# Kernel optimization log

Hardware: AMD Instinct MI355X
Metric: run time of the kernel (lower is better)

The kernel has to match this reference:

```python
import jax, jax.numpy as jnp
import numpy as np

N = 50000
E = 1600000
IN = 128
HID = 128
OUT = 64
NEG_SLOPE = 0.2  # DGL GATConv default leaky_relu slope


def _gat_layer(h, src, dst, W, al, ar, b, res=None, act=True):
    """DGL GATConv layer on an edge-list graph.
    h: [N, F_in]; W: [F_in, H*D]; al, ar, b: [H, D]; res: None | [N,H,D].
    Returns [N, H, D].
    """
    H, D = al.shape
    f = (h @ W).reshape(N, H, D)                      # fc projection
    el = jnp.sum(f * al, axis=-1)                     # [N, H]
    er = jnp.sum(f * ar, axis=-1)                     # [N, H]
    e = jax.nn.leaky_relu(el[src] + er[dst], NEG_SLOPE)  # [E, H]
    # edge softmax over incoming edges of each dst node
    m = jax.ops.segment_max(e, dst, num_segments=N)   # [N, H]
    ex = jnp.exp(e - m[dst])                          # [E, H]
    s = jax.ops.segment_sum(ex, dst, num_segments=N)  # [N, H]
    alpha = ex / s[dst]                               # [E, H]
    msg = f[src] * alpha[..., None]                   # [E, H, D]
    rst = jax.ops.segment_sum(msg, dst, num_segments=N)  # [N, H, D]
    if res is not None:
        rst = rst + res
    rst = rst + b                                     # bias [H, D] broadcast
    if act:
        rst = jax.nn.elu(rst)
    return rst


def setup_inputs() -> dict:
    key = jax.random.key(0)
    ks = jax.random.split(key, 16)
    x = jax.random.normal(ks[0], (N, IN), dtype=jnp.float32)
    src = jax.random.randint(ks[1], (E,), 0, N)
    dst = jax.random.randint(ks[2], (E,), 0, N)
    sc = 0.05
    # layer 0: IN -> 8 heads x 16, no residual, elu
    W0 = jax.random.normal(ks[3], (IN, 8 * 16), dtype=jnp.float32) * sc
    al0 = jax.random.normal(ks[4], (8, 16), dtype=jnp.float32) * sc
    ar0 = jax.random.normal(ks[5], (8, 16), dtype=jnp.float32) * sc
    b0 = jnp.zeros((8, 16), dtype=jnp.float32)
    # layer 1: HID -> 8 heads x 16, identity residual (HID == 8*16), elu
    W1 = jax.random.normal(ks[6], (HID, 8 * 16), dtype=jnp.float32) * sc
    al1 = jax.random.normal(ks[7], (8, 16), dtype=jnp.float32) * sc
    ar1 = jax.random.normal(ks[8], (8, 16), dtype=jnp.float32) * sc
    b1 = jnp.zeros((8, 16), dtype=jnp.float32)
    # layer 2: HID -> 1 head x 64, linear residual (128 != 64), no act
    W2 = jax.random.normal(ks[9], (HID, 1 * OUT), dtype=jnp.float32) * sc
    al2 = jax.random.normal(ks[10], (1, OUT), dtype=jnp.float32) * sc
    ar2 = jax.random.normal(ks[11], (1, OUT), dtype=jnp.float32) * sc
    b2 = jnp.zeros((1, OUT), dtype=jnp.float32)
    resW2 = jax.random.normal(ks[12], (HID, 1 * OUT), dtype=jnp.float32) * sc
    return {"x": x, "src": src, "dst": dst,
            "W0": W0, "al0": al0, "ar0": ar0, "b0": b0,
            "W1": W1, "al1": al1, "ar1": ar1, "b1": b1,
            "W2": W2, "al2": al2, "ar2": ar2, "b2": b2,
            "resW2": resW2}


def reference(x, src, dst, W0, al0, ar0, b0, W1, al1, ar1, b1,
              W2, al2, ar2, b2, resW2):
    # layer 0: no residual, elu, flatten heads (dropout=0)
    h = _gat_layer(x, src, dst, W0, al0, ar0, b0, res=None, act=True)
    h = h.reshape(N, -1)  # [N, 128]
    # layer 1: identity residual, elu, flatten heads
    res1 = h.reshape(N, 8, 16)
    h = _gat_layer(h, src, dst, W1, al1, ar1, b1, res=res1, act=True)
    h = h.reshape(N, -1)  # [N, 128]
    # layer 2: linear residual, no activation, mean over heads
    res2 = (h @ resW2).reshape(N, 1, OUT)
    h = _gat_layer(h, src, dst, W2, al2, ar2, b2, res=res2, act=False)
    return h.mean(axis=1)  # [N, 64]
```

## Files before the change

kernel.cpp:

```cpp
#include <hip/hip_runtime.h>
#include <hip/hip_fp16.h>
#include <math.h>


#define GN 50000
#define GE 1600000
#define NB 391
#define NBLK_A 512
#define CHUNK 3125

typedef _Float16 half8 __attribute__((ext_vector_type(8)));
typedef _Float16 half4v __attribute__((ext_vector_type(4)));
typedef float f32x4 __attribute__((ext_vector_type(4)));


__global__ __launch_bounds__(256) void bucketA(const int* __restrict__ dst, int* __restrict__ cnt) {
    __shared__ int hist[NB];
    for (int i = threadIdx.x; i < NB; i += 256) hist[i] = 0;
    __syncthreads();
    int b = blockIdx.x;
    int beg = b * CHUNK, end = beg + CHUNK;
    for (int i = beg + threadIdx.x; i < end; i += 256)
        atomicAdd(&hist[dst[i] >> 7], 1);
    __syncthreads();
    for (int k = threadIdx.x; k < NB; k += 256)
        cnt[k * NBLK_A + b] = hist[k];
}

__global__ __launch_bounds__(512) void bucketB(int* __restrict__ cnt, int* __restrict__ tot) {
    __shared__ int s[512];
    int k = blockIdx.x, t = threadIdx.x;
    int* row = cnt + k * NBLK_A;
    s[t] = row[t];
    __syncthreads();
    for (int ofs = 1; ofs < 512; ofs <<= 1) {
        int v = (t >= ofs) ? s[t - ofs] : 0;
        __syncthreads();
        s[t] += v;
        __syncthreads();
    }
    row[t] = (t == 0) ? 0 : s[t - 1];
    if (t == 511) tot[k] = s[511];
}

__global__ __launch_bounds__(512) void bucketB2(const int* __restrict__ tot, int* __restrict__ base,
                                                int* __restrict__ offs) {
    __shared__ int s[512];
    int t = threadIdx.x;
    s[t] = (t < NB) ? tot[t] : 0;
    __syncthreads();
    for (int ofs = 1; ofs < 512; ofs <<= 1) {
        int v = (t >= ofs) ? s[t - ofs] : 0;
        __syncthreads();
        s[t] += v;
        __syncthreads();
    }
    if (t <= NB) base[t] = (t == 0) ? 0 : s[t - 1];
    if (t == 0) offs[GN] = GE;
}

__global__ __launch_bounds__(256) void bucketC(const int* __restrict__ src, const int* __restrict__ dst,
                                               const int* __restrict__ cnt, const int* __restrict__ base,
                                               unsigned* __restrict__ ebuf) {
    __shared__ int cur[NB];
    int b = blockIdx.x;
    for (int k = threadIdx.x; k < NB; k += 256)
        cur[k] = base[k] + cnt[k * NBLK_A + b];
    __syncthreads();
    int beg = b * CHUNK, end = beg + CHUNK;
    for (int i = beg + threadIdx.x; i < end; i += 256) {
        int d = dst[i];
        int pos = atomicAdd(&cur[d >> 7], 1);
        ebuf[pos] = (unsigned)src[i] | ((unsigned)(d & 127) << 16);
    }
}

__global__ __launch_bounds__(256) void bucketD(const unsigned* __restrict__ ebuf, const int* __restrict__ base,
                                               int* __restrict__ offs, int* __restrict__ csrc) {
    __shared__ int hist[128], pre[128], cur[128];
    int k = blockIdx.x, t = threadIdx.x;
    if (t < 128) hist[t] = 0;
    __syncthreads();
    int lo = base[k], hi = base[k + 1];
    for (int i = lo + t; i < hi; i += 256)
        atomicAdd(&hist[ebuf[i] >> 16], 1);
    __syncthreads();
    if (t < 128) pre[t] = hist[t];
    __syncthreads();
    for (int ofs = 1; ofs < 128; ofs <<= 1) {
        int v = 0;
        if (t < 128 && t >= ofs) v = pre[t - ofs];
        __syncthreads();
        if (t < 128) pre[t] += v;
        __syncthreads();
    }
    if (t < 128) {
        int excl = (t == 0) ? 0 : pre[t - 1];
        cur[t] = lo + excl;
        int node = (k << 7) + t;
        if (node < GN) offs[node] = lo + excl;
    }
    __syncthreads();
    for (int i = lo + t; i < hi; i += 256) {
        unsigned v = ebuf[i];
        int pos = atomicAdd(&cur[v >> 16], 1);
        csrc[pos] = (int)(v & 0xFFFFu);
    }
}


__global__ __launch_bounds__(256) void wt_ker(const float* __restrict__ W, _Float16* __restrict__ WT, int N) {
    int i = blockIdx.x * 256 + threadIdx.x;
    if (i >= N * 128) return;
    int n = i >> 7, k = i & 127;
    WT[i] = (_Float16)W[k * N + n];
}

__global__ __launch_bounds__(256) void cvt_ker(const float4* __restrict__ X, __half2* __restrict__ Y, int n4) {
    int i = blockIdx.x * 256 + threadIdx.x;
    if (i >= n4) return;
    float4 v = X[i];
    Y[i * 2]     = __floats2half2_rn(v.x, v.y);
    Y[i * 2 + 1] = __floats2half2_rn(v.z, v.w);
}


template <int NT>
__global__ __launch_bounds__(256) void gemm_mfma(const _Float16* __restrict__ A,
                                                 const _Float16* __restrict__ WT,
                                                 _Float16* __restrict__ C, int nrows) {
    const int N = NT * 16;
    int wave = threadIdx.x >> 6;
    int lane = threadIdx.x & 63;
    int quad = lane >> 4;
    int l16 = lane & 15;
    int m = blockIdx.x * 64 + wave * 16 + l16;
    int mc = (m < nrows) ? m : (nrows - 1);
    const _Float16* ap = A + (size_t)mc * 128 + quad * 8;
    half8 a[4];
    #pragma unroll
    for (int kk = 0; kk < 4; ++kk) a[kk] = *(const half8*)(ap + kk * 32);
    f32x4 acc[NT];
    #pragma unroll
    for (int nt = 0; nt < NT; ++nt) acc[nt] = (f32x4){0.f, 0.f, 0.f, 0.f};
    const _Float16* wp = WT + (size_t)l16 * 128 + quad * 8;
    #pragma unroll
    for (int nt = 0; nt < NT; ++nt) {
        #pragma unroll
        for (int kk = 0; kk < 4; ++kk) {
            half8 b = *(const half8*)(wp + nt * 16 * 128 + kk * 32);
            acc[nt] = __builtin_amdgcn_mfma_f32_16x16x32_f16(a[kk], b, acc[nt], 0, 0, 0);
        }
    }
    int row0 = blockIdx.x * 64 + wave * 16 + quad * 4;
    #pragma unroll
    for (int nt = 0; nt < NT; ++nt) {
        #pragma unroll
        for (int r = 0; r < 4; ++r) {
            int row = row0 + r;
            if (row < nrows) C[(size_t)row * N + nt * 16 + l16] = (_Float16)acc[nt][r];
        }
    }
}


template <int H, int D>
__global__ __launch_bounds__(256) void attn_ker(const __half* __restrict__ f, const float* __restrict__ al,
                                                const float* __restrict__ ar, float* __restrict__ el,
                                                float* __restrict__ er, int total) {
    int i = blockIdx.x * 256 + threadIdx.x;
    if (i >= total) return;
    int h = i % H;
    const __half2* fp = (const __half2*)(f + (size_t)i * D);
    const float2* alp = (const float2*)(al + h * D);
    const float2* arp = (const float2*)(ar + h * D);
    float sl = 0.f, sr = 0.f;
    #pragma unroll
    for (int d = 0; d < D / 2; ++d) {
        float2 fv = __half22float2(fp[d]);
        float2 av = alp[d];
        float2 rv = arp[d];
        sl += fv.x * av.x + fv.y * av.y;
        sr += fv.x * rv.x + fv.y * rv.y;
    }
    el[i] = sl;
    er[i] = sr;
}


__global__ __launch_bounds__(256) void agg_multi(const int* __restrict__ offs, const int* __restrict__ csrc,
                                                 const _Float16* __restrict__ fh, const float* __restrict__ el,
                                                 const float* __restrict__ er, const float* __restrict__ bias,
                                                 const _Float16* __restrict__ resid, _Float16* __restrict__ out,
                                                 int n) {
    int node = blockIdx.x * 16 + (threadIdx.x >> 4);
    int lg = threadIdx.x & 15;
    if (node >= n) return;
    int head = lg >> 1;
    float ern = er[node * 8 + head];
    int beg = offs[node], end = offs[node + 1];
    float acc[8] = {};
    float ssum = 0.f;
    int e = beg;
    for (; e + 4 <= end; e += 4) {
        int s0 = csrc[e], s1 = csrc[e + 1], s2 = csrc[e + 2], s3 = csrc[e + 3];
        float e0 = el[s0 * 8 + head] + ern;
        float e1 = el[s1 * 8 + head] + ern;
        float e2 = el[s2 * 8 + head] + ern;
        float e3 = el[s3 * 8 + head] + ern;
        half8 q0 = *(const half8*)(fh + (size_t)s0 * 128 + lg * 8);
        half8 q1 = *(const half8*)(fh + (size_t)s1 * 128 + lg * 8);
        half8 q2 = *(const half8*)(fh + (size_t)s2 * 128 + lg * 8);
        half8 q3 = *(const half8*)(fh + (size_t)s3 * 128 + lg * 8);
        e0 = fmaxf(e0, 0.2f * e0);
        e1 = fmaxf(e1, 0.2f * e1);
        e2 = fmaxf(e2, 0.2f * e2);
        e3 = fmaxf(e3, 0.2f * e3);
        float w0 = __expf(e0), w1 = __expf(e1), w2 = __expf(e2), w3 = __expf(e3);
        ssum += (w0 + w1) + (w2 + w3);
        #pragma unroll
        for (int j = 0; j < 8; ++j)
            acc[j] += w0 * (float)q0[j] + w1 * (float)q1[j]
                    + w2 * (float)q2[j] + w3 * (float)q3[j];
    }
    for (; e < end; ++e) {
        int s = csrc[e];
        float ev = el[s * 8 + head] + ern;
        ev = fmaxf(ev, 0.2f * ev);
        float w = __expf(ev);
        half8 q = *(const half8*)(fh + (size_t)s * 128 + lg * 8);
        ssum += w;
        #pragma unroll
        for (int j = 0; j < 8; ++j) acc[j] += w * (float)q[j];
    }
    float inv = (ssum > 0.f) ? 1.0f / ssum : 0.f;
    float o[8];
    #pragma unroll
    for (int j = 0; j < 8; ++j) o[j] = acc[j] * inv + bias[lg * 8 + j];
    if (resid) {
        half8 r = *(const half8*)(resid + (size_t)node * 128 + lg * 8);
        #pragma unroll
        for (int j = 0; j < 8; ++j) o[j] += (float)r[j];
    }
    half8 ov;
    #pragma unroll
    for (int j = 0; j < 8; ++j) {
        float v = o[j];
        v = (v > 0.f) ? v : expm1f(v);
        ov[j] = (_Float16)v;
    }
    *(half8*)(out + (size_t)node * 128 + lg * 8) = ov;
}

__global__ __launch_bounds__(256) void agg_single(const int* __restrict__ offs, const int* __restrict__ csrc,
                                                  const _Float16* __restrict__ fh, const float* __restrict__ el,
                                                  const float* __restrict__ er, const float* __restrict__ bias,
                                                  const _Float16* __restrict__ resid, float* __restrict__ out,
                                                  int n) {
    int node = blockIdx.x * 16 + (threadIdx.x >> 4);
    int lg = threadIdx.x & 15;
    if (node >= n) return;
    float ern = er[node];
    int beg = offs[node], end = offs[node + 1];
    float acc[4] = {};
    float ssum = 0.f;
    int e = beg;
    for (; e + 4 <= end; e += 4) {
        int s0 = csrc[e], s1 = csrc[e + 1], s2 = csrc[e + 2], s3 = csrc[e + 3];
        float e0 = el[s0] + ern;
        float e1 = el[s1] + ern;
        float e2 = el[s2] + ern;
        float e3 = el[s3] + ern;
        half4v q0 = *(const half4v*)(fh + (size_t)s0 * 64 + lg * 4);
        half4v q1 = *(const half4v*)(fh + (size_t)s1 * 64 + lg * 4);
        half4v q2 = *(const half4v*)(fh + (size_t)s2 * 64 + lg * 4);
        half4v q3 = *(const half4v*)(fh + (size_t)s3 * 64 + lg * 4);
        e0 = fmaxf(e0, 0.2f * e0);
        e1 = fmaxf(e1, 0.2f * e1);
        e2 = fmaxf(e2, 0.2f * e2);
        e3 = fmaxf(e3, 0.2f * e3);
        float w0 = __expf(e0), w1 = __expf(e1), w2 = __expf(e2), w3 = __expf(e3);
        ssum += (w0 + w1) + (w2 + w3);
        #pragma unroll
        for (int j = 0; j < 4; ++j)
            acc[j] += w0 * (float)q0[j] + w1 * (float)q1[j]
                    + w2 * (float)q2[j] + w3 * (float)q3[j];
    }
    for (; e < end; ++e) {
        int s = csrc[e];
        float ev = el[s] + ern;
        ev = fmaxf(ev, 0.2f * ev);
        float w = __expf(ev);
        half4v q = *(const half4v*)(fh + (size_t)s * 64 + lg * 4);
        ssum += w;
        #pragma unroll
        for (int j = 0; j < 4; ++j) acc[j] += w * (float)q[j];
    }
    float inv = (ssum > 0.f) ? 1.0f / ssum : 0.f;
    half4v r = *(const half4v*)(resid + (size_t)node * 64 + lg * 4);
    float4 o;
    o.x = acc[0] * inv + bias[lg * 4 + 0] + (float)r[0];
    o.y = acc[1] * inv + bias[lg * 4 + 1] + (float)r[1];
    o.z = acc[2] * inv + bias[lg * 4 + 2] + (float)r[2];
    o.w = acc[3] * inv + bias[lg * 4 + 3] + (float)r[3];
    *(float4*)(out + (size_t)node * 64 + lg * 4) = o;
}


extern "C" void kernel_launch(void* const* d_in, const int* in_sizes, int n_in,
                              void* d_out, int out_size, void* d_ws, size_t ws_size,
                              hipStream_t stream) {
    const float* x     = (const float*)d_in[0];
    const int*   src   = (const int*)d_in[1];
    const int*   dst   = (const int*)d_in[2];
    const float* W0    = (const float*)d_in[3];
    const float* al0   = (const float*)d_in[4];
    const float* ar0   = (const float*)d_in[5];
    const float* b0    = (const float*)d_in[6];
    const float* W1    = (const float*)d_in[7];
    const float* al1   = (const float*)d_in[8];
    const float* ar1   = (const float*)d_in[9];
    const float* b1    = (const float*)d_in[10];
    const float* W2    = (const float*)d_in[11];
    const float* al2   = (const float*)d_in[12];
    const float* ar2   = (const float*)d_in[13];
    const float* b2    = (const float*)d_in[14];
    const float* resW2 = (const float*)d_in[15];
    float* out = (float*)d_out;

    char* w = (char*)d_ws;
    auto alloc = [&](size_t bytes) {
        char* p = w;
        w += (bytes + 255) & ~(size_t)255;
        return p;
    };
    int*      base  = (int*)alloc((size_t)(NB + 1) * 4);
    int*      offs  = (int*)alloc((size_t)(GN + 1) * 4);
    int*      csrc  = (int*)alloc((size_t)GE * 4);
    _Float16* fbuf  = (_Float16*)alloc((size_t)GN * 128 * 2);
    float*    elb   = (float*)alloc((size_t)GN * 8 * 4);
    float*    erb   = (float*)alloc((size_t)GN * 8 * 4);
    _Float16* x16   = (_Float16*)alloc((size_t)GN * 128 * 2);
    _Float16* hA    = (_Float16*)alloc((size_t)GN * 128 * 2);
    _Float16* hB    = (_Float16*)alloc((size_t)GN * 128 * 2);
    _Float16* res2  = (_Float16*)alloc((size_t)GN * 64 * 2);
    _Float16* w0t   = (_Float16*)alloc(128 * 128 * 2);
    _Float16* w1t   = (_Float16*)alloc(128 * 128 * 2);
    _Float16* w2t   = (_Float16*)alloc(64 * 128 * 2);
    _Float16* rw2t  = (_Float16*)alloc(64 * 128 * 2);

    int*      cnt  = (int*)hA;
    int*      tot  = (int*)hA + NB * NBLK_A;
    unsigned* ebuf = (unsigned*)hB;

    bucketA<<<NBLK_A, 256, 0, stream>>>(dst, cnt);
    bucketB<<<NB, 512, 0, stream>>>(cnt, tot);
    bucketB2<<<1, 512, 0, stream>>>(tot, base, offs);
    bucketC<<<NBLK_A, 256, 0, stream>>>(src, dst, cnt, base, ebuf);
    bucketD<<<NB, 256, 0, stream>>>(ebuf, base, offs, csrc);

    wt_ker<<<(128 * 128 + 255) / 256, 256, 0, stream>>>(W0, w0t, 128);
    wt_ker<<<(128 * 128 + 255) / 256, 256, 0, stream>>>(W1, w1t, 128);
    wt_ker<<<(64 * 128 + 255) / 256, 256, 0, stream>>>(W2, w2t, 64);
    wt_ker<<<(64 * 128 + 255) / 256, 256, 0, stream>>>(resW2, rw2t, 64);
    cvt_ker<<<(GN * 32 + 255) / 256, 256, 0, stream>>>((const float4*)x, (__half2*)x16, GN * 32);

    dim3 gblk(256);
    int gemmGrid = (GN + 63) / 64;
    int aggGrid = (GN + 15) / 16;

    gemm_mfma<8><<<gemmGrid, gblk, 0, stream>>>(x16, w0t, fbuf, GN);
    attn_ker<8, 16><<<(GN * 8 + 255) / 256, gblk, 0, stream>>>((const __half*)fbuf, al0, ar0, elb, erb, GN * 8);
    agg_multi<<<aggGrid, gblk, 0, stream>>>(offs, csrc, fbuf, elb, erb, b0, nullptr, hA, GN);

    gemm_mfma<8><<<gemmGrid, gblk, 0, stream>>>(hA, w1t, fbuf, GN);
    attn_ker<8, 16><<<(GN * 8 + 255) / 256, gblk, 0, stream>>>((const __half*)fbuf, al1, ar1, elb, erb, GN * 8);
    agg_multi<<<aggGrid, gblk, 0, stream>>>(offs, csrc, fbuf, elb, erb, b1, hA, hB, GN);

    gemm_mfma<4><<<gemmGrid, gblk, 0, stream>>>(hB, w2t, fbuf, GN);
    gemm_mfma<4><<<gemmGrid, gblk, 0, stream>>>(hB, rw2t, res2, GN);
    attn_ker<1, 64><<<(GN + 255) / 256, gblk, 0, stream>>>((const __half*)fbuf, al2, ar2, elb, erb, GN);
    agg_single<<<aggGrid, gblk, 0, stream>>>(offs, csrc, fbuf, elb, erb, b2, res2, out, GN);
}
```

Before: 402.9 us.

## Fuse attention-score computation and fp32 input conversion into MFMA projection GEMMs

Each layer's projection GEMM now also computes el/er with an extra MFMA. It stages the fp16 output tile in shared memory and multiplies it by a block-diagonal attention matrix built once in a combined prep kernel. Layer 0 reads fp32 x directly and converts it in registers, which drops the separate conversion pass and the x16 buffer. Layer 2's two GEMMs (projection and residual) share one A load in a dual variant. Together this removes several kernel launches and full re-reads of the feature buffers, at the cost of more LDS and registers per GEMM block and attention logits computed from fp16-rounded features and weights.

```diff
diff --git a/kernel.cpp b/kernel.cpp
--- a/kernel.cpp
+++ b/kernel.cpp
@@ -109,82 +109,145 @@
 }
 
 
-__global__ __launch_bounds__(256) void wt_ker(const float* __restrict__ W, _Float16* __restrict__ WT, int N) {
+__global__ __launch_bounds__(256) void prep(const float* __restrict__ W0, const float* __restrict__ W1,
+                                            const float* __restrict__ W2, const float* __restrict__ rW2,
+                                            const float* __restrict__ al0, const float* __restrict__ ar0,
+                                            const float* __restrict__ al1, const float* __restrict__ ar1,
+                                            const float* __restrict__ al2, const float* __restrict__ ar2,
+                                            _Float16* __restrict__ w0t, _Float16* __restrict__ w1t,
+                                            _Float16* __restrict__ w2t, _Float16* __restrict__ rw2t,
+                                            _Float16* __restrict__ aB0, _Float16* __restrict__ aB1,
+                                            _Float16* __restrict__ aB2) {
     int i = blockIdx.x * 256 + threadIdx.x;
-    if (i >= N * 128) return;
-    int n = i >> 7, k = i & 127;
-    WT[i] = (_Float16)W[k * N + n];
-}
-
-__global__ __launch_bounds__(256) void cvt_ker(const float4* __restrict__ X, __half2* __restrict__ Y, int n4) {
-    int i = blockIdx.x * 256 + threadIdx.x;
-    if (i >= n4) return;
-    float4 v = X[i];
-    Y[i * 2]     = __floats2half2_rn(v.x, v.y);
-    Y[i * 2 + 1] = __floats2half2_rn(v.z, v.w);
-}
-
-
-template <int NT>
-__global__ __launch_bounds__(256) void gemm_mfma(const _Float16* __restrict__ A,
-                                                 const _Float16* __restrict__ WT,
-                                                 _Float16* __restrict__ C, int nrows) {
+    if (i < 16384) {
+        int n = i >> 7, k = i & 127;
+        w0t[i] = (_Float16)W0[k * 128 + n];
+        w1t[i] = (_Float16)W1[k * 128 + n];
+    }
+    if (i < 8192) {
+        int n = i >> 7, k = i & 127;
+        w2t[i] = (_Float16)W2[k * 64 + n];
+        rw2t[i] = (_Float16)rW2[k * 64 + n];
+    }
+    if (i < 2048) {
+        int n = i >> 7, k = i & 127;
+        _Float16 v0 = (_Float16)0.f, v1 = (_Float16)0.f, v2 = (_Float16)0.f;
+        if (n < 8) {
+            if ((k >> 4) == n) {
+                v0 = (_Float16)al0[n * 16 + (k & 15)];
+                v1 = (_Float16)al1[n * 16 + (k & 15)];
+            }
+        } else {
+            int h = n - 8;
+            if ((k >> 4) == h) {
+                v0 = (_Float16)ar0[h * 16 + (k & 15)];
+                v1 = (_Float16)ar1[h * 16 + (k & 15)];
+            }
+        }
+        if (n == 0 && k < 64) v2 = (_Float16)al2[k];
+        if (n == 1 && k < 64) v2 = (_Float16)ar2[k];
+        aB0[i] = v0; aB1[i] = v1; aB2[i] = v2;
+    }
+}
+
+
+template <int NT, bool AF32, bool DUAL, bool MULTI>
+__global__ __launch_bounds__(256) void gemm_att(const void* __restrict__ Av,
+                                                const _Float16* __restrict__ WT,
+                                                const _Float16* __restrict__ WT2,
+                                                const _Float16* __restrict__ attB,
+                                                _Float16* __restrict__ C, _Float16* __restrict__ C2,
+                                                float* __restrict__ elb, float* __restrict__ erb,
+                                                int nrows) {
     const int N = NT * 16;
-    int wave = threadIdx.x >> 6;
-    int lane = threadIdx.x & 63;
-    int quad = lane >> 4;
-    int l16 = lane & 15;
+    __shared__ _Float16 lt[4][16][NT * 16 + 4];
+    int wave = threadIdx.x >> 6, lane = threadIdx.x & 63;
+    int quad = lane >> 4, l16 = lane & 15;
     int m = blockIdx.x * 64 + wave * 16 + l16;
     int mc = (m < nrows) ? m : (nrows - 1);
-    const _Float16* ap = A + (size_t)mc * 128 + quad * 8;
     half8 a[4];
-    #pragma unroll
-    for (int kk = 0; kk < 4; ++kk) a[kk] = *(const half8*)(ap + kk * 32);
+    if (AF32) {
+        const float* ap = (const float*)Av + (size_t)mc * 128 + quad * 8;
+        #pragma unroll
+        for (int kk = 0; kk < 4; ++kk) {
+            float4 u = *(const float4*)(ap + kk * 32);
+            float4 v = *(const float4*)(ap + kk * 32 + 4);
+            half8 t;
+            t[0] = (_Float16)u.x; t[1] = (_Float16)u.y; t[2] = (_Float16)u.z; t[3] = (_Float16)u.w;
+            t[4] = (_Float16)v.x; t[5] = (_Float16)v.y; t[6] = (_Float16)v.z; t[7] = (_Float16)v.w;
+            a[kk] = t;
+        }
+    } else {
+        const _Float16* ap = (const _Float16*)Av + (size_t)mc * 128 + quad * 8;
+        #pragma unroll
+        for (int kk = 0; kk < 4; ++kk) a[kk] = *(const half8*)(ap + kk * 32);
+    }
     f32x4 acc[NT];
+    f32x4 acc2[DUAL ? NT : 1];
     #pragma unroll
     for (int nt = 0; nt < NT; ++nt) acc[nt] = (f32x4){0.f, 0.f, 0.f, 0.f};
+    if (DUAL) {
+        #pragma unroll
+        for (int nt = 0; nt < NT; ++nt) acc2[nt] = (f32x4){0.f, 0.f, 0.f, 0.f};
+    }
     const _Float16* wp = WT + (size_t)l16 * 128 + quad * 8;
+    const _Float16* wp2 = DUAL ? (WT2 + (size_t)l16 * 128 + quad * 8) : WT;
     #pragma unroll
     for (int nt = 0; nt < NT; ++nt) {
         #pragma unroll
         for (int kk = 0; kk < 4; ++kk) {
             half8 b = *(const half8*)(wp + nt * 16 * 128 + kk * 32);
             acc[nt] = __builtin_amdgcn_mfma_f32_16x16x32_f16(a[kk], b, acc[nt], 0, 0, 0);
+            if (DUAL) {
+                half8 b2 = *(const half8*)(wp2 + nt * 16 * 128 + kk * 32);
+                acc2[nt] = __builtin_amdgcn_mfma_f32_16x16x32_f16(a[kk], b2, acc2[nt], 0, 0, 0);
+            }
         }
     }
     int row0 = blockIdx.x * 64 + wave * 16 + quad * 4;
     #pragma unroll
     for (int nt = 0; nt < NT; ++nt) {
+        #pragma unroll
+        for (int r = 0; r < 4; ++r) {
+            _Float16 hv = (_Float16)acc[nt][r];
+            lt[wave][quad * 4 + r][nt * 16 + l16] = hv;
+            int row = row0 + r;
+            if (row < nrows) {
+                C[(size_t)row * N + nt * 16 + l16] = hv;
+                if (DUAL) C2[(size_t)row * N + nt * 16 + l16] = (_Float16)acc2[nt][r];
+            }
+        }
+    }
+    f32x4 att = {0.f, 0.f, 0.f, 0.f};
+    const _Float16* bp = attB + (size_t)l16 * 128 + quad * 8;
+    constexpr int KCH = (NT == 8) ? 4 : 2;
+    #pragma unroll
+    for (int kk = 0; kk < KCH; ++kk) {
+        const _Float16* lp = &lt[wave][l16][kk * 32 + quad * 8];
+        half4v lo = *(const half4v*)lp;
+        half4v hi = *(const half4v*)(lp + 4);
+        half8 af = __builtin_shufflevector(lo, hi, 0, 1, 2, 3, 4, 5, 6, 7);
+        half8 bf = *(const half8*)(bp + kk * 32);
+        att = __builtin_amdgcn_mfma_f32_16x16x32_f16(af, bf, att, 0, 0, 0);
+    }
+    if (MULTI) {
+        int hh = l16 & 7;
+        float* dstp = (l16 < 8) ? elb : erb;
         #pragma unroll
         for (int r = 0; r < 4; ++r) {
             int row = row0 + r;
-            if (row < nrows) C[(size_t)row * N + nt * 16 + l16] = (_Float16)acc[nt][r];
-        }
-    }
-}
-
-
-template <int H, int D>
-__global__ __launch_bounds__(256) void attn_ker(const __half* __restrict__ f, const float* __restrict__ al,
-                                                const float* __restrict__ ar, float* __restrict__ el,
-                                                float* __restrict__ er, int total) {
-    int i = blockIdx.x * 256 + threadIdx.x;
-    if (i >= total) return;
-    int h = i % H;
-    const __half2* fp = (const __half2*)(f + (size_t)i * D);
-    const float2* alp = (const float2*)(al + h * D);
-    const float2* arp = (const float2*)(ar + h * D);
-    float sl = 0.f, sr = 0.f;
-    #pragma unroll
-    for (int d = 0; d < D / 2; ++d) {
-        float2 fv = __half22float2(fp[d]);
-        float2 av = alp[d];
-        float2 rv = arp[d];
-        sl += fv.x * av.x + fv.y * av.y;
-        sr += fv.x * rv.x + fv.y * rv.y;
-    }
-    el[i] = sl;
-    er[i] = sr;
+            if (row < nrows) dstp[row * 8 + hh] = att[r];
+        }
+    } else {
+        if (l16 < 2) {
+            float* dstp = (l16 == 0) ? elb : erb;
+            #pragma unroll
+            for (int r = 0; r < 4; ++r) {
+                int row = row0 + r;
+                if (row < nrows) dstp[row] = att[r];
+            }
+        }
+    }
 }
 
 
@@ -340,7 +403,6 @@
     _Float16* fbuf  = (_Float16*)alloc((size_t)GN * 128 * 2);
     float*    elb   = (float*)alloc((size_t)GN * 8 * 4);
     float*    erb   = (float*)alloc((size_t)GN * 8 * 4);
-    _Float16* x16   = (_Float16*)alloc((size_t)GN * 128 * 2);
     _Float16* hA    = (_Float16*)alloc((size_t)GN * 128 * 2);
     _Float16* hB    = (_Float16*)alloc((size_t)GN * 128 * 2);
     _Float16* res2  = (_Float16*)alloc((size_t)GN * 64 * 2);
@@ -348,6 +410,9 @@
     _Float16* w1t   = (_Float16*)alloc(128 * 128 * 2);
     _Float16* w2t   = (_Float16*)alloc(64 * 128 * 2);
     _Float16* rw2t  = (_Float16*)alloc(64 * 128 * 2);
+    _Float16* aB0   = (_Float16*)alloc(16 * 128 * 2);
+    _Float16* aB1   = (_Float16*)alloc(16 * 128 * 2);
+    _Float16* aB2   = (_Float16*)alloc(16 * 128 * 2);
 
     int*      cnt  = (int*)hA;
     int*      tot  = (int*)hA + NB * NBLK_A;
@@ -359,26 +424,22 @@
     bucketC<<<NBLK_A, 256, 0, stream>>>(src, dst, cnt, base, ebuf);
     bucketD<<<NB, 256, 0, stream>>>(ebuf, base, offs, csrc);
 
-    wt_ker<<<(128 * 128 + 255) / 256, 256, 0, stream>>>(W0, w0t, 128);
-    wt_ker<<<(128 * 128 + 255) / 256, 256, 0, stream>>>(W1, w1t, 128);
-    wt_ker<<<(64 * 128 + 255) / 256, 256, 0, stream>>>(W2, w2t, 64);
-    wt_ker<<<(64 * 128 + 255) / 256, 256, 0, stream>>>(resW2, rw2t, 64);
-    cvt_ker<<<(GN * 32 + 255) / 256, 256, 0, stream>>>((const float4*)x, (__half2*)x16, GN * 32);
+    prep<<<64, 256, 0, stream>>>(W0, W1, W2, resW2, al0, ar0, al1, ar1, al2, ar2,
+                                 w0t, w1t, w2t, rw2t, aB0, aB1, aB2);
 
     dim3 gblk(256);
     int gemmGrid = (GN + 63) / 64;
     int aggGrid = (GN + 15) / 16;
 
-    gemm_mfma<8><<<gemmGrid, gblk, 0, stream>>>(x16, w0t, fbuf, GN);
-    attn_ker<8, 16><<<(GN * 8 + 255) / 256, gblk, 0, stream>>>((const __half*)fbuf, al0, ar0, elb, erb, GN * 8);
+    gemm_att<8, true, false, true><<<gemmGrid, gblk, 0, stream>>>(
+        x, w0t, nullptr, aB0, fbuf, nullptr, elb, erb, GN);
     agg_multi<<<aggGrid, gblk, 0, stream>>>(offs, csrc, fbuf, elb, erb, b0, nullptr, hA, GN);
 
-    gemm_mfma<8><<<gemmGrid, gblk, 0, stream>>>(hA, w1t, fbuf, GN);
-    attn_ker<8, 16><<<(GN * 8 + 255) / 256, gblk, 0, stream>>>((const __half*)fbuf, al1, ar1, elb, erb, GN * 8);
+    gemm_att<8, false, false, true><<<gemmGrid, gblk, 0, stream>>>(
+        hA, w1t, nullptr, aB1, fbuf, nullptr, elb, erb, GN);
     agg_multi<<<aggGrid, gblk, 0, stream>>>(offs, csrc, fbuf, elb, erb, b1, hA, hB, GN);
 
-    gemm_mfma<4><<<gemmGrid, gblk, 0, stream>>>(hB, w2t, fbuf, GN);
-    gemm_mfma<4><<<gemmGrid, gblk, 0, stream>>>(hB, rw2t, res2, GN);
-    attn_ker<1, 64><<<(GN + 255) / 256, gblk, 0, stream>>>((const __half*)fbuf, al2, ar2, elb, erb, GN);
+    gemm_att<4, false, true, false><<<gemmGrid, gblk, 0, stream>>>(
+        hB, w2t, rw2t, aB2, fbuf, res2, elb, erb, GN);
     agg_single<<<aggGrid, gblk, 0, stream>>>(offs, csrc, fbuf, elb, erb, b2, res2, out, GN);
 }
```

New measurement: 387.9 us. 1.04x faster.
